# Kernel tuning notes

Hardware: AMD Instinct MI355X
Metric: run time of the kernel (lower is better)

## Reference

```python
import jax, jax.numpy as jnp
import numpy as np
import math

IMAGE_SIZE = 300
STEPS = [16, 32, 64, 100, 150, 300]
MIN_SIZES = [60, 105, 150, 195, 240, 285]
MAX_SIZES = [105, 150, 195, 240, 285, 330]
ASPECT_RATIOS = [2, 3]
SCORE_THRESH = 0.02
NMS_THRESH = 0.45
POST_NMS_TOP_N = 100
VAR_XY, VAR_WH = 0.1, 0.2
BATCH, NUM_CLASSES = 16, 201


def _make_priors():
    # SSD-style anchor generation in (cx, cy, w, h), relative coords.
    priors = []
    for k, step in enumerate(STEPS):
        f = math.ceil(IMAGE_SIZE / step)
        s = MIN_SIZES[k] / IMAGE_SIZE
        sp = math.sqrt(MIN_SIZES[k] * MAX_SIZES[k]) / IMAGE_SIZE
        for i in range(f):
            for j in range(f):
                cx = (j + 0.5) * step / IMAGE_SIZE
                cy = (i + 0.5) * step / IMAGE_SIZE
                priors.append([cx, cy, s, s])
                priors.append([cx, cy, sp, sp])
                for ar in ASPECT_RATIOS:
                    r = math.sqrt(ar)
                    priors.append([cx, cy, s * r, s / r])
                    priors.append([cx, cy, s / r, s * r])
    return np.asarray(priors, dtype=np.float32)  # [3000, 4]


def setup_inputs() -> dict:
    key = jax.random.key(0)
    k1, k2 = jax.random.split(key)
    priors = jnp.asarray(_make_priors())  # [P, 4]
    P = priors.shape[0]
    pred_bbox_deltas = jax.random.normal(k1, (BATCH, P, 4), dtype=jnp.float32)
    objectness = jax.random.normal(k2, (BATCH, P, NUM_CLASSES), dtype=jnp.float32)
    return {"pred_bbox_deltas": pred_bbox_deltas, "objectness": objectness, "priors": priors}


def reference(pred_bbox_deltas, objectness, priors):
    # Eval path of MultiBoxHeads.filter_priors: softmax -> box decode ->
    # score filter -> class-aware (batched) NMS -> top-N, padded to fixed size.
    P = priors.shape[0]
    C = objectness.shape[-1]
    probs = jax.nn.softmax(objectness, axis=-1)  # [B, P, C]

    # BoxCoder.decode with variances (0.1, 0.2); priors are (cx, cy, w, h).
    pxy, pwh = priors[:, :2], priors[:, 2:]
    xy = pred_bbox_deltas[..., :2] * VAR_XY * pwh + pxy  # [B, P, 2]
    wh = jnp.exp(pred_bbox_deltas[..., 2:] * VAR_WH) * pwh
    decoded = jnp.concatenate([xy - 0.5 * wh, xy + 0.5 * wh], axis=-1)  # [B, P, 4] xyxy

    # Per-candidate class labels (background class 0 dropped), shared across images.
    labels = jnp.broadcast_to(jnp.arange(1, C), (P, C - 1)).reshape(-1)  # [P*(C-1)] int

    def nms_image(dec, prob):
        scores = prob[:, 1:].reshape(-1)  # [P*(C-1)]
        boxes = jnp.broadcast_to(dec[:, None, :], (P, C - 1, 4)).reshape(-1, 4)
        s = jnp.where(scores > SCORE_THRESH, scores, -1.0)
        # batched_nms trick: offset boxes by label so classes never overlap.
        off = jnp.max(boxes) + 1.0
        bo = boxes + labels.astype(boxes.dtype)[:, None] * off
        areas = (bo[:, 2] - bo[:, 0]) * (bo[:, 3] - bo[:, 1])

        def step(s, _):
            i = jnp.argmax(s)
            sc = s[i]
            b = bo[i]
            ix1 = jnp.maximum(bo[:, 0], b[0])
            iy1 = jnp.maximum(bo[:, 1], b[1])
            ix2 = jnp.minimum(bo[:, 2], b[2])
            iy2 = jnp.minimum(bo[:, 3], b[3])
            inter = jnp.clip(ix2 - ix1, 0.0) * jnp.clip(iy2 - iy1, 0.0)
            iou = inter / (areas + areas[i] - inter)
            s = jnp.where(iou > NMS_THRESH, -1.0, s).at[i].set(-1.0)
            return s, (i, sc)

        _, (idx, sc) = jax.lax.scan(step, s, None, length=POST_NMS_TOP_N)
        ok = sc > SCORE_THRESH  # slots that hold real detections
        b_out = jnp.where(ok[:, None], jnp.clip(boxes[idx], 0.0, 1.0), 0.0)  # parse() clamp
        s_out = jnp.where(ok, sc, 0.0)
        l_out = jnp.where(ok, labels[idx].astype(boxes.dtype), 0.0)
        # [K, 6] = (x1, y1, x2, y2, score, label); zero rows are padding.
        return jnp.concatenate([b_out, s_out[:, None], l_out[:, None]], axis=-1)

    return jax.vmap(nms_image)(decoded, probs)  # [B, POST_NMS_TOP_N, 6]
```

## Files before the change

kernel.cpp:

```cpp
#include <hip/hip_runtime.h>
#include <cfloat>
#include <cstdint>

#define BATCH 16
#define PRIORS 3000
#define NCLS 201
#define NLBL 200
#define TOPN 100
#define SCORE_THR 0.02f
#define NMS_THR 0.45f

#define FPPB 16
#define FBLK ((PRIORS + FPPB - 1) / FPPB)
#define SEGW 64
#define SEGS (FBLK * 4)
#define SLOTS (SEGS * SEGW)
#define HOTW 8
#define OVF_CAP 1024
#define T0 0.08f

#define NMS_T 1024
#define NBINS 1024
#define HCAP 512
#define SB_BASE 0x3CA3

__device__ __forceinline__ int key_stratum(uint64_t k) {
    int s = (int)(k >> 48) - SB_BASE;
    return s < 0 ? 0 : (s > NBINS - 1 ? NBINS - 1 : s);
}

__global__ __launch_bounds__(256) void score_filter_kernel(
    const float* __restrict__ obj,
    int*         __restrict__ cnt,
    int*         __restrict__ hcnt,
    uint64_t*    __restrict__ seg,
    uint64_t*    __restrict__ hot,
    uint64_t*    __restrict__ ovf,
    uint64_t*    __restrict__ hovf)
{
    const int b    = blockIdx.y;
    const int wave = threadIdx.x >> 6;
    const int lane = threadIdx.x & 63;
    const int segId = blockIdx.x * 4 + wave;
    uint64_t* myseg = seg + ((size_t)b * SEGS + segId) * SEGW;
    uint64_t* myhot = hot + ((size_t)b * SEGS + segId) * HOTW;
    const int pbase = blockIdx.x * FPPB + wave * 4;

    float v0[4], v1[4], v2[4], v3[4];
    bool pv[4];
#pragma unroll
    for (int pp = 0; pp < 4; ++pp) {
        int p = pbase + pp;
        pv[pp] = (p < PRIORS);
        const float* x = obj + ((size_t)b * PRIORS + (pv[pp] ? p : PRIORS - 1)) * NCLS;
        v0[pp] = x[lane];
        v1[pp] = x[lane + 64];
        v2[pp] = x[lane + 128];
        v3[pp] = (lane + 192 < NCLS) ? x[lane + 192] : -FLT_MAX;
    }
    float mx[4];
#pragma unroll
    for (int pp = 0; pp < 4; ++pp)
        mx[pp] = fmaxf(fmaxf(v0[pp], v1[pp]), fmaxf(v2[pp], v3[pp]));
    for (int d = 32; d > 0; d >>= 1) {
#pragma unroll
        for (int pp = 0; pp < 4; ++pp)
            mx[pp] = fmaxf(mx[pp], __shfl_xor(mx[pp], d, 64));
    }
    float e0[4], e1[4], e2[4], e3[4], se[4];
#pragma unroll
    for (int pp = 0; pp < 4; ++pp) {
        e0[pp] = expf(v0[pp] - mx[pp]);
        e1[pp] = expf(v1[pp] - mx[pp]);
        e2[pp] = expf(v2[pp] - mx[pp]);
        e3[pp] = (lane + 192 < NCLS) ? expf(v3[pp] - mx[pp]) : 0.0f;
        se[pp] = e0[pp] + e1[pp] + e2[pp] + e3[pp];
    }
    for (int d = 32; d > 0; d >>= 1) {
#pragma unroll
        for (int pp = 0; pp < 4; ++pp)
            se[pp] += __shfl_xor(se[pp], d, 64);
    }
    int cursor = 0, hcur = 0;
#pragma unroll
    for (int pp = 0; pp < 4; ++pp) {
        float inv = 1.0f / se[pp];
        int p = pbase + pp;
        float ev[4] = { e0[pp], e1[pp], e2[pp], e3[pp] };
#pragma unroll
        for (int k = 0; k < 4; ++k) {
            int c = lane + 64 * k;
            float prob = ev[k] * inv;
            bool pass = pv[pp] && (c >= 1) && (c < NCLS) && (prob > SCORE_THR);
            uint64_t mask = __ballot(pass);
            bool hotp = pass && (prob > T0);
            uint64_t hmask = __ballot(hotp);
            if (pass) {
                uint32_t oid = (uint32_t)(p * NLBL + (c - 1));
                uint64_t key = ((uint64_t)__float_as_uint(prob) << 32)
                             | (uint64_t)(0xFFFFFFFFu - oid);
                int idx = cursor + __popcll(mask & ((1ull << lane) - 1ull));
                if (idx < SEGW) {
                    myseg[idx] = key;
                } else {
                    int gi = atomicAdd(&cnt[b], 1);
                    if (gi < OVF_CAP) ovf[(size_t)b * OVF_CAP + gi] = key;
                }
                if (hotp) {
                    int hidx = hcur + __popcll(hmask & ((1ull << lane) - 1ull));
                    if (hidx < HOTW) {
                        myhot[hidx] = key;
                    } else {
                        int gi = atomicAdd(&hcnt[b], 1);
                        if (gi < OVF_CAP) hovf[(size_t)b * OVF_CAP + gi] = key;
                    }
                }
            }
            cursor += (int)__popcll(mask);
            hcur   += (int)__popcll(hmask);
        }
    }
    if (lane >= (cursor < SEGW ? cursor : SEGW)) myseg[lane] = 0ull;
    if (lane < HOTW && lane >= (hcur < HOTW ? hcur : HOTW)) myhot[lane] = 0ull;
}

__device__ __forceinline__ void sort512_desc(const uint64_t* skey,
                                             uint64_t K[8], int lane)
{
#pragma unroll
    for (int r = 0; r < 8; ++r) K[r] = skey[r * 64 + lane];
#pragma unroll
    for (int k2 = 2; k2 <= 512; k2 <<= 1) {
#pragma unroll
        for (int j2 = k2 >> 1; j2 >= 64; j2 >>= 1) {
            int j2r = j2 >> 6;
#pragma unroll
            for (int r = 0; r < 8; ++r) {
                if ((r & j2r) == 0) {
                    int rp = r | j2r;
                    bool up = ((((r << 6) + lane) & k2) == 0);
                    uint64_t a = K[r], bb = K[rp];
                    uint64_t mxk = a > bb ? a : bb;
                    uint64_t mnk = a > bb ? bb : a;
                    K[r]  = up ? mxk : mnk;
                    K[rp] = up ? mnk : mxk;
                }
            }
        }
#pragma unroll
        for (int j2 = ((k2 >> 1) < 32 ? (k2 >> 1) : 32); j2 >= 1; j2 >>= 1) {
#pragma unroll
            for (int r = 0; r < 8; ++r) {
                uint64_t o = __shfl_xor((unsigned long long)K[r], j2, 64);
                bool up = ((((r << 6) + lane) & k2) == 0);
                bool lower = ((lane & j2) == 0);
                K[r] = (up == lower) ? (K[r] > o ? K[r] : o)
                                     : (K[r] < o ? K[r] : o);
            }
        }
    }
}

__device__ __forceinline__ int scan_sorted_w0(
    const uint64_t K[8], int b, const float4* __restrict__ dbox, float ofb,
    float4* abox, float* aarea, int na, float* __restrict__ out, int lane)
{
#pragma unroll
    for (int r = 0; r < 8; ++r) {
        if (na >= TOPN) break;
        uint64_t myk = K[r];
        bool valid = (myk != 0ull);
        uint32_t oid = 0xFFFFFFFFu - (uint32_t)myk;
        int p = valid ? (int)(oid / NLBL) : 0;
        int c = valid ? ((int)(oid - (uint32_t)p * NLBL) + 1) : 1;
        float4 db = dbox[p];
        float lof = (float)c * ofb;
        float qx1 = db.x + lof, qy1 = db.y + lof;
        float qx2 = db.z + lof, qy2 = db.w + lof;
        float aq = (qx2 - qx1) * (qy2 - qy1);
        bool dead = false;
        for (int l = 0; l < na; ++l) {
            float4 a = abox[l];
            float ix1 = fmaxf(qx1, a.x), iy1 = fmaxf(qy1, a.y);
            float ix2 = fminf(qx2, a.z), iy2 = fminf(qy2, a.w);
            float inter = fmaxf(ix2 - ix1, 0.0f) * fmaxf(iy2 - iy1, 0.0f);
            float iou = inter / (aq + aarea[l] - inter);
            if (iou > NMS_THR) dead = true;
        }
        uint64_t alive = __ballot(valid && !dead);
        while (alive != 0ull && na < TOPN) {
            int j = __ffsll((unsigned long long)alive) - 1;
            float ax1 = __shfl(qx1, j, 64);
            float ay1 = __shfl(qy1, j, 64);
            float ax2 = __shfl(qx2, j, 64);
            float ay2 = __shfl(qy2, j, 64);
            float aa  = __shfl(aq,  j, 64);
            if (lane == j) {
                abox[na]  = make_float4(qx1, qy1, qx2, qy2);
                aarea[na] = aq;
                float* o = out + ((size_t)b * TOPN + na) * 6;
                o[0] = fminf(fmaxf(db.x, 0.0f), 1.0f);
                o[1] = fminf(fmaxf(db.y, 0.0f), 1.0f);
                o[2] = fminf(fmaxf(db.z, 0.0f), 1.0f);
                o[3] = fminf(fmaxf(db.w, 0.0f), 1.0f);
                o[4] = __uint_as_float((uint32_t)(myk >> 32));
                o[5] = (float)c;
            }
            na++;
            bool mine = ((alive >> lane) & 1ull) != 0ull;
            bool drop = (lane == j);
            if (mine && !drop) {
                float ix1 = fmaxf(qx1, ax1), iy1 = fmaxf(qy1, ay1);
                float ix2 = fminf(qx2, ax2), iy2 = fminf(qy2, ay2);
                float inter = fmaxf(ix2 - ix1, 0.0f) * fmaxf(iy2 - iy1, 0.0f);
                float iou = inter / (aq + aa - inter);
                if (iou > NMS_THR) drop = true;
            }
            alive = __ballot(mine && !drop);
        }
    }
    return na;
}

__device__ __forceinline__ int scan_step_w0(
    uint64_t key, int b, const float4* __restrict__ dbox, float ofb,
    float4* abox, float* aarea, int na, float* __restrict__ out, int lane)
{
    uint32_t oid = 0xFFFFFFFFu - (uint32_t)key;
    int p = (int)(oid / NLBL);
    int c = (int)(oid - (uint32_t)p * NLBL) + 1;
    float4 db = dbox[p];
    float lo = (float)c * ofb;
    float qx1 = db.x + lo, qy1 = db.y + lo;
    float qx2 = db.z + lo, qy2 = db.w + lo;
    float aq = (qx2 - qx1) * (qy2 - qy1);
    bool sup = false;
    for (int l = lane; l < na; l += 64) {
        float4 a = abox[l];
        float ix1 = fmaxf(qx1, a.x), iy1 = fmaxf(qy1, a.y);
        float ix2 = fminf(qx2, a.z), iy2 = fminf(qy2, a.w);
        float inter = fmaxf(ix2 - ix1, 0.0f) * fmaxf(iy2 - iy1, 0.0f);
        float iou = inter / (aq + aarea[l] - inter);
        if (iou > NMS_THR) sup = true;
    }
    if (__ballot(sup) == 0ull) {
        if (lane == 0) {
            abox[na]  = make_float4(qx1, qy1, qx2, qy2);
            aarea[na] = aq;
            float* o = out + ((size_t)b * TOPN + na) * 6;
            o[0] = fminf(fmaxf(db.x, 0.0f), 1.0f);
            o[1] = fminf(fmaxf(db.y, 0.0f), 1.0f);
            o[2] = fminf(fmaxf(db.z, 0.0f), 1.0f);
            o[3] = fminf(fmaxf(db.w, 0.0f), 1.0f);
            o[4] = __uint_as_float((uint32_t)(key >> 32));
            o[5] = (float)c;
        }
        __threadfence_block();
        return na + 1;
    }
    return na;
}

__global__ __launch_bounds__(NMS_T) void nms_kernel(
    const float*    __restrict__ deltas,
    const float*    __restrict__ priors,
    const int*      __restrict__ cnt,
    const int*      __restrict__ hcnt,
    const uint64_t* __restrict__ seg,
    const uint64_t* __restrict__ hot,
    const uint64_t* __restrict__ ovf,
    const uint64_t* __restrict__ hovf,
    float*          __restrict__ out)
{
    __shared__ float4   dbox[PRIORS];
    __shared__ int      sufx[NBINS];
    __shared__ uint64_t skey[HCAP];
    __shared__ float4   qbox[HCAP];
    __shared__ float    qarea[HCAP];
    __shared__ uint64_t adj[HCAP * 8];
    __shared__ float4   abox[112];
    __shared__ float    aarea[112];
    __shared__ uint64_t rk[NMS_T / 64];
    __shared__ float    wredF[NMS_T / 64];
    __shared__ int      wtotS[NMS_T / 64];
    __shared__ int      carryS[NMS_T / 64];
    __shared__ int cntC, loS, naS;
    __shared__ uint64_t fkS;

    const int b    = blockIdx.x;
    const int tid  = threadIdx.x;
    const int wave = tid >> 6;
    const int lane = tid & 63;
    const uint64_t* slots  = seg  + (size_t)b * SLOTS;
    const uint64_t* hslots = hot  + (size_t)b * SEGS * HOTW;
    int n_ovf  = cnt[b];  if (n_ovf  > OVF_CAP) n_ovf  = OVF_CAP;
    int n_hovf = hcnt[b]; if (n_hovf > OVF_CAP) n_hovf = OVF_CAP;
    const uint64_t* ovfp  = ovf  + (size_t)b * OVF_CAP;
    const uint64_t* hovfp = hovf + (size_t)b * OVF_CAP;

    if (tid == 0) { cntC = 0; naS = 0; }
    if (lane == 0) wredF[wave] = -FLT_MAX;
    __syncthreads();

    for (int j = tid; j < SEGS * HOTW; j += NMS_T) {
        uint64_t k = hslots[j];
        if (k) { int i = atomicAdd(&cntC, 1); if (i < HCAP) skey[i] = k; }
    }
    for (int j = tid; j < n_hovf; j += NMS_T) {
        uint64_t k = hovfp[j];
        if (k) { int i = atomicAdd(&cntC, 1); if (i < HCAP) skey[i] = k; }
    }
    __syncthreads();
    int hc = cntC;
    bool decoded = false;
    if (hc <= HCAP) {
        if (tid < HCAP && tid >= hc) skey[tid] = 0ull;
        __syncthreads();
        if (wave == 0) {
            uint64_t K[8];
            sort512_desc(skey, K, lane);
#pragma unroll
            for (int r = 0; r < 8; ++r) skey[r * 64 + lane] = K[r];
        } else {
            int base0 = (wave - 1) * 200;
            float lmax = -FLT_MAX;
            for (int p = base0 + lane; p < base0 + 200; p += 64) {
                float4 d4 = ((const float4*)deltas)[(size_t)b * PRIORS + p];
                float4 pr = ((const float4*)priors)[p];
                float cx = d4.x * 0.1f * pr.z + pr.x;
                float cy = d4.y * 0.1f * pr.w + pr.y;
                float w  = expf(d4.z * 0.2f) * pr.z;
                float h  = expf(d4.w * 0.2f) * pr.w;
                float x1 = cx - 0.5f * w, y1 = cy - 0.5f * h;
                float x2 = cx + 0.5f * w, y2 = cy + 0.5f * h;
                dbox[p] = make_float4(x1, y1, x2, y2);
                lmax = fmaxf(lmax, fmaxf(fmaxf(x1, y1), fmaxf(x2, y2)));
            }
            for (int d = 32; d > 0; d >>= 1)
                lmax = fmaxf(lmax, __shfl_xor(lmax, d, 64));
            if (lane == 0) wredF[wave] = lmax;
        }
        decoded = true;
        __syncthreads();

        float v = wredF[lane & 15];
        for (int d = 8; d > 0; d >>= 1) v = fmaxf(v, __shfl_xor(v, d, 64));
        float ofb = v + 1.0f;

        if (tid < HCAP) {
            uint64_t k = skey[tid];
            bool valid = (k != 0ull);
            uint32_t oid = 0xFFFFFFFFu - (uint32_t)k;
            int p = valid ? (int)(oid / NLBL) : 0;
            int c = valid ? ((int)(oid - (uint32_t)p * NLBL) + 1) : 1;
            float4 db = dbox[p];
            float lof = (float)c * ofb;
            float4 q = make_float4(db.x + lof, db.y + lof,
                                   db.z + lof, db.w + lof);
            qbox[tid]  = q;
            qarea[tid] = (q.z - q.x) * (q.w - q.y);
        }
        for (int i = tid; i < HCAP * 8; i += NMS_T) adj[i] = 0ull;
        __syncthreads();

        int hcw = (hc + 63) >> 6;
        int P2  = (hcw * (hcw + 1)) >> 1;
        for (int tau = tid; tau < (P2 << 6); tau += NMS_T) {
            int pair = tau >> 6, rr = tau & 63;
            int w = 0;
            while ((((w + 1) * (w + 2)) >> 1) <= pair) ++w;
            int cw = pair - ((w * (w + 1)) >> 1);
            int r  = (cw << 6) + rr;
            float4 qr = qbox[r];
            float  ar = qarea[r];
            int jb = w << 6;
            uint64_t m = 0ull;
#pragma unroll 8
            for (int j = 0; j < 64; ++j) {
                float4 qj = qbox[jb + j];
                float ix1 = fmaxf(qr.x, qj.x), iy1 = fmaxf(qr.y, qj.y);
                float ix2 = fminf(qr.z, qj.z), iy2 = fminf(qr.w, qj.w);
                float inter = fmaxf(ix2 - ix1, 0.0f) * fmaxf(iy2 - iy1, 0.0f);
                float iou = inter / (ar + qarea[jb + j] - inter);
                m |= (uint64_t)(iou > NMS_THR) << j;
            }
            if (w == cw) m &= ~((1ull << rr) - 1ull);
            adj[(r << 3) + w] = m;
        }
        __syncthreads();

        if (wave == 0) {
            uint64_t alive = 0ull;
            if (lane < 8) {
                int n = hc - (lane << 6);
                alive = (n >= 64) ? ~0ull : (n > 0 ? ((1ull << n) - 1ull) : 0ull);
            }
            int na = 0;
            while (na < TOPN) {
                uint64_t nz = __ballot((lane < 8) && (alive != 0ull));
                if (nz == 0ull) break;
                int w0 = __ffsll((unsigned long long)nz) - 1;
                uint64_t aw = (uint64_t)__shfl((long long)alive, w0, 64);
                int r = (w0 << 6) + __ffsll((unsigned long long)aw) - 1;
                if (lane < 8) alive &= ~adj[(r << 3) + lane];
                if (lane == 8) {
                    uint64_t myk = skey[r];
                    uint32_t oid = 0xFFFFFFFFu - (uint32_t)myk;
                    int p = (int)(oid / NLBL);
                    int c = (int)(oid - (uint32_t)p * NLBL) + 1;
                    float4 db = dbox[p];
                    float* o = out + ((size_t)b * TOPN + na) * 6;
                    o[0] = fminf(fmaxf(db.x, 0.0f), 1.0f);
                    o[1] = fminf(fmaxf(db.y, 0.0f), 1.0f);
                    o[2] = fminf(fmaxf(db.z, 0.0f), 1.0f);
                    o[3] = fminf(fmaxf(db.w, 0.0f), 1.0f);
                    o[4] = __uint_as_float((uint32_t)(myk >> 32));
                    o[5] = (float)c;
                }
                ++na;
            }
            if (lane == 0) naS = na;
        }
        __syncthreads();
    }

    if (naS < TOPN) {
        if (!decoded) {
            float lmax = -FLT_MAX;
            for (int p = tid; p < PRIORS; p += NMS_T) {
                float4 d4 = ((const float4*)deltas)[(size_t)b * PRIORS + p];
                float4 pr = ((const float4*)priors)[p];
                float cx = d4.x * 0.1f * pr.z + pr.x;
                float cy = d4.y * 0.1f * pr.w + pr.y;
                float w  = expf(d4.z * 0.2f) * pr.z;
                float h  = expf(d4.w * 0.2f) * pr.w;
                float x1 = cx - 0.5f * w, y1 = cy - 0.5f * h;
                float x2 = cx + 0.5f * w, y2 = cy + 0.5f * h;
                dbox[p] = make_float4(x1, y1, x2, y2);
                lmax = fmaxf(lmax, fmaxf(fmaxf(x1, y1), fmaxf(x2, y2)));
            }
            for (int d = 32; d > 0; d >>= 1)
                lmax = fmaxf(lmax, __shfl_xor(lmax, d, 64));
            if (lane == 0) wredF[wave] = lmax;
        }
        sufx[tid] = 0;
        if (tid == 0) naS = 0;
        __syncthreads();
        for (int j = tid; j < SLOTS; j += NMS_T) {
            uint64_t k = slots[j];
            if (k) atomicAdd(&sufx[key_stratum(k)], 1);
        }
        for (int j = tid; j < n_ovf; j += NMS_T) {
            uint64_t k = ovfp[j];
            if (k) atomicAdd(&sufx[key_stratum(k)], 1);
        }
        __syncthreads();
        {
            int v = sufx[64 * wave + lane];
            int s = v;
            for (int d = 1; d < 64; d <<= 1) {
                int t = __shfl_down(s, d, 64);
                if (lane + d < 64) s += t;
            }
            if (lane == 0) wtotS[wave] = s;
            __syncthreads();
            if (wave == 0 && lane < NMS_T / 64) {
                int tv = wtotS[lane];
                int ts = tv;
                for (int d = 1; d < NMS_T / 64; d <<= 1) {
                    int t = __shfl_down(ts, d, 64);
                    if (lane + d < NMS_T / 64) ts += t;
                }
                carryS[lane] = ts - tv;
            }
            __syncthreads();
            sufx[64 * wave + lane] = s + carryS[wave];
        }
        int curHi = NBINS;
        for (;;) {
            __syncthreads();
            int naCur = naS;
            int A = (curHi < NBINS) ? sufx[curHi] : 0;
            int remaining = sufx[0] - A;
            if (naCur >= TOPN || remaining <= 0 || curHi <= 0) break;
            int target = A + HCAP;
            if (tid == 0) { loS = curHi; cntC = 0; }
            __syncthreads();
            if (tid < curHi) {
                if (sufx[tid] <= target && (tid == 0 || sufx[tid - 1] > target))
                    loS = tid;
            }
            __syncthreads();
            int lo = loS;

            if (lo < curHi) {
                for (int j = tid; j < SLOTS; j += NMS_T) {
                    uint64_t k = slots[j];
                    if (k) {
                        int s = key_stratum(k);
                        if (s >= lo && s < curHi) {
                            int i = atomicAdd(&cntC, 1);
                            if (i < HCAP) skey[i] = k;
                        }
                    }
                }
                for (int j = tid; j < n_ovf; j += NMS_T) {
                    uint64_t k = ovfp[j];
                    if (k) {
                        int s = key_stratum(k);
                        if (s >= lo && s < curHi) {
                            int i = atomicAdd(&cntC, 1);
                            if (i < HCAP) skey[i] = k;
                        }
                    }
                }
                __syncthreads();
                if (tid < HCAP && tid >= cntC) skey[tid] = 0ull;
                __syncthreads();
                if (wave == 0) {
                    uint64_t K[8];
                    sort512_desc(skey, K, lane);
                    float ofb;
                    {
                        float v = (lane < NMS_T / 64) ? wredF[lane] : -FLT_MAX;
                        for (int d = 32; d > 0; d >>= 1) v = fmaxf(v, __shfl_xor(v, d, 64));
                        ofb = v + 1.0f;
                    }
                    int na = scan_sorted_w0(K, b, dbox, ofb, abox, aarea, naS, out, lane);
                    if (lane == 0) naS = na;
                }
                curHi = lo;
            } else {
                float ofbT;
                {
                    float v = (lane < NMS_T / 64) ? wredF[lane] : -FLT_MAX;
                    for (int d = 32; d > 0; d >>= 1) v = fmaxf(v, __shfl_xor(v, d, 64));
                    ofbT = v + 1.0f;
                }
                int s = curHi - 1;
                uint64_t lastK = ~0ull;
                for (;;) {
                    __syncthreads();
                    if (naS >= TOPN) break;
                    uint64_t bk = 0ull;
                    for (int j = tid; j < SLOTS; j += NMS_T) {
                        uint64_t k = slots[j];
                        if (k && key_stratum(k) == s && k < lastK && k > bk) bk = k;
                    }
                    for (int j = tid; j < n_ovf; j += NMS_T) {
                        uint64_t k = ovfp[j];
                        if (k && key_stratum(k) == s && k < lastK && k > bk) bk = k;
                    }
                    for (int d = 32; d > 0; d >>= 1) {
                        uint64_t o = __shfl_xor((unsigned long long)bk, d, 64);
                        bk = (o > bk) ? o : bk;
                    }
                    if (lane == 0) rk[wave] = bk;
                    __syncthreads();
                    if (tid == 0) {
                        uint64_t fk = rk[0];
                        for (int w = 1; w < NMS_T / 64; ++w) fk = (rk[w] > fk) ? rk[w] : fk;
                        fkS = fk;
                    }
                    __syncthreads();
                    uint64_t fk = fkS;
                    if (fk == 0ull) break;
                    if (wave == 0) {
                        int nal = naS;
                        nal = scan_step_w0(fk, b, dbox, ofbT, abox, aarea, nal, out, lane);
                        if (lane == 0) naS = nal;
                    }
                    lastK = fk;
                }
                curHi = s;
            }
        }
    }
    __syncthreads();
    int naF = naS;
    for (int idx = tid; idx < (TOPN - naF) * 6; idx += NMS_T)
        out[(size_t)b * TOPN * 6 + (size_t)naF * 6 + idx] = 0.0f;
}

extern "C" void kernel_launch(void* const* d_in, const int* in_sizes, int n_in,
                              void* d_out, int out_size, void* d_ws, size_t ws_size,
                              hipStream_t stream)
{
    const float* deltas = (const float*)d_in[0];
    const float* obj    = (const float*)d_in[1];
    const float* priors = (const float*)d_in[2];
    float* out = (float*)d_out;

    char* ws = (char*)d_ws;
    int*      cnt  = (int*)ws;
    int*      hcnt = (int*)(ws + 64);
    uint64_t* hotA = (uint64_t*)(ws + 256);
    uint64_t* segA = hotA + (size_t)BATCH * SEGS * HOTW;
    uint64_t* ovfA = segA + (size_t)BATCH * SLOTS;
    uint64_t* hovA = ovfA + (size_t)BATCH * OVF_CAP;

    hipMemsetAsync(ws, 0, 128, stream);
    dim3 fg(FBLK, BATCH, 1);
    score_filter_kernel<<<fg, 256, 0, stream>>>(obj, cnt, hcnt, segA, hotA, ovfA, hovA);
    nms_kernel<<<BATCH, NMS_T, 0, stream>>>(deltas, priors, cnt, hcnt,
                                            segA, hotA, ovfA, hovA, out);
}
```

Measured before the change: 147.5 us.

## Transpose NMS adjacency and defer output writes to parallel scatter

The suppression bitmask matrix is stored word-major with padding, so the serial greedy scan can process one 64-candidate word at a time. It updates a local remaining-mask using only the diagonal word and carries the suppression of later words in lanes 8-15. Output rows are no longer written by a single lane inside the serial loop. The loop records the kept bits per word, and afterwards up to 512 threads compute each kept row's index with popcounts and write it in parallel. This shortens the serial critical path (fewer ballots and shuffles, no global stores per iteration) at the cost of an extra barrier and a scatter phase.

```diff
diff --git a/kernel.cpp b/kernel.cpp
--- a/kernel.cpp
+++ b/kernel.cpp
@@ -22,6 +22,7 @@
 #define NMS_T 1024
 #define NBINS 1024
 #define HCAP 512
+#define ADJS 514
 #define SB_BASE 0x3CA3
 
 __device__ __forceinline__ int key_stratum(uint64_t k) {
@@ -277,7 +278,7 @@
     __shared__ uint64_t skey[HCAP];
     __shared__ float4   qbox[HCAP];
     __shared__ float    qarea[HCAP];
-    __shared__ uint64_t adj[HCAP * 8];
+    __shared__ uint64_t adjT[8 * ADJS];
     __shared__ float4   abox[112];
     __shared__ float    aarea[112];
     __shared__ uint64_t rk[NMS_T / 64];
@@ -360,7 +361,7 @@
             qbox[tid]  = q;
             qarea[tid] = (q.z - q.x) * (q.w - q.y);
         }
-        for (int i = tid; i < HCAP * 8; i += NMS_T) adj[i] = 0ull;
+        for (int i = tid; i < 8 * ADJS; i += NMS_T) adjT[i] = 0ull;
         __syncthreads();
 
         int hcw = (hc + 63) >> 6;
@@ -385,41 +386,57 @@
                 m |= (uint64_t)(iou > NMS_THR) << j;
             }
             if (w == cw) m &= ~((1ull << rr) - 1ull);
-            adj[(r << 3) + w] = m;
-        }
+            adjT[w * ADJS + r] = m;
+        }
+        if (wave == 0 && lane < 8) rk[lane] = 0ull;
         __syncthreads();
 
         if (wave == 0) {
-            uint64_t alive = 0ull;
-            if (lane < 8) {
-                int n = hc - (lane << 6);
-                alive = (n >= 64) ? ~0ull : (n > 0 ? ((1ull << n) - 1ull) : 0ull);
-            }
+            uint64_t sup = 0ull;
             int na = 0;
-            while (na < TOPN) {
-                uint64_t nz = __ballot((lane < 8) && (alive != 0ull));
-                if (nz == 0ull) break;
-                int w0 = __ffsll((unsigned long long)nz) - 1;
-                uint64_t aw = (uint64_t)__shfl((long long)alive, w0, 64);
-                int r = (w0 << 6) + __ffsll((unsigned long long)aw) - 1;
-                if (lane < 8) alive &= ~adj[(r << 3) + lane];
-                if (lane == 8) {
-                    uint64_t myk = skey[r];
-                    uint32_t oid = 0xFFFFFFFFu - (uint32_t)myk;
-                    int p = (int)(oid / NLBL);
-                    int c = (int)(oid - (uint32_t)p * NLBL) + 1;
-                    float4 db = dbox[p];
-                    float* o = out + ((size_t)b * TOPN + na) * 6;
-                    o[0] = fminf(fmaxf(db.x, 0.0f), 1.0f);
-                    o[1] = fminf(fmaxf(db.y, 0.0f), 1.0f);
-                    o[2] = fminf(fmaxf(db.z, 0.0f), 1.0f);
-                    o[3] = fminf(fmaxf(db.w, 0.0f), 1.0f);
-                    o[4] = __uint_as_float((uint32_t)(myk >> 32));
-                    o[5] = (float)c;
-                }
-                ++na;
+            for (int w = 0; w < hcw && na < TOPN; ++w) {
+                int nInW = hc - (w << 6);
+                uint64_t init = (nInW >= 64) ? ~0ull
+                              : (nInW > 0 ? ((1ull << nInW) - 1ull) : 0ull);
+                uint64_t supw = (uint64_t)__shfl((long long)sup, 8 + w, 64);
+                uint64_t rem  = init & ~supw;
+                uint64_t accw = 0ull;
+                while (rem != 0ull && na < TOPN) {
+                    int rr = __ffsll((unsigned long long)rem) - 1;
+                    int r  = (w << 6) + rr;
+                    accw |= 1ull << rr;
+                    uint64_t rowk = 0ull;
+                    if (lane >= 8 && lane < 16)
+                        rowk = adjT[(lane - 8) * ADJS + r];
+                    sup |= rowk;
+                    rem &= ~adjT[w * ADJS + r];
+                    ++na;
+                }
+                if (lane == 0) rk[w] = accw;
             }
             if (lane == 0) naS = na;
+        }
+        __syncthreads();
+
+        if (tid < HCAP) {
+            int w = tid >> 6, rr = tid & 63;
+            uint64_t aw = rk[w];
+            if ((aw >> rr) & 1ull) {
+                int idx = (int)__popcll(aw & ((1ull << rr) - 1ull));
+                for (int k = 0; k < w; ++k) idx += (int)__popcll(rk[k]);
+                uint64_t myk = skey[tid];
+                uint32_t oid = 0xFFFFFFFFu - (uint32_t)myk;
+                int p = (int)(oid / NLBL);
+                int c = (int)(oid - (uint32_t)p * NLBL) + 1;
+                float4 db = dbox[p];
+                float* o = out + ((size_t)b * TOPN + idx) * 6;
+                o[0] = fminf(fmaxf(db.x, 0.0f), 1.0f);
+                o[1] = fminf(fmaxf(db.y, 0.0f), 1.0f);
+                o[2] = fminf(fmaxf(db.z, 0.0f), 1.0f);
+                o[3] = fminf(fmaxf(db.w, 0.0f), 1.0f);
+                o[4] = __uint_as_float((uint32_t)(myk >> 32));
+                o[5] = (float)c;
+            }
         }
         __syncthreads();
     }
```

Result: faster. 134.0 us (-9.1%).
